# Kernel tuning notes

Measured on AMD Instinct MI355X. Metric: run time of the kernel, lower is better.

## Reference

```python
import jax, jax.numpy as jnp
import numpy as np

B, D, DP, H = 65536, 512, 256, 8
HD = D // H  # head dim = 64
EPS = 1e-5


def _layernorm(x, gamma, beta):
    mu = jnp.mean(x, axis=-1, keepdims=True)
    var = jnp.var(x, axis=-1, keepdims=True)
    return (x - mu) * jax.lax.rsqrt(var + EPS) * gamma + beta


def setup_inputs() -> dict:
    key = jax.random.key(0)
    ks = jax.random.split(key, 16)
    n = lambda k, shape, s=0.02: (jax.random.normal(k, shape, jnp.float32) * s)
    return {
        "cell_emb": jax.random.normal(ks[0], (B, D), jnp.float32),
        "pert_emb": jax.random.normal(ks[1], (B, DP), jnp.float32),
        # perturbation_proj: Linear(DP -> D)
        "Wp": n(ks[2], (D, DP)), "bp": jnp.zeros((D,), jnp.float32),
        # MultiheadAttention in/out projections (each D x D)
        "Wq": n(ks[3], (D, D)), "bq": jnp.zeros((D,), jnp.float32),
        "Wk": n(ks[4], (D, D)), "bk": jnp.zeros((D,), jnp.float32),
        "Wv": n(ks[5], (D, D)), "bv": jnp.zeros((D,), jnp.float32),
        "Wo": n(ks[6], (D, D)), "bo": jnp.zeros((D,), jnp.float32),
        # norm1, norm2
        "g1": jnp.ones((D,), jnp.float32), "be1": jnp.zeros((D,), jnp.float32),
        "g2": jnp.ones((D,), jnp.float32), "be2": jnp.zeros((D,), jnp.float32),
        # FFN: Linear(D -> 2D), GELU, Linear(2D -> D)
        "W1": n(ks[7], (2 * D, D)), "b1": jnp.zeros((2 * D,), jnp.float32),
        "W2": n(ks[8], (D, 2 * D)), "b2": jnp.zeros((D,), jnp.float32),
    }


def reference(cell_emb, pert_emb, Wp, bp, Wq, bq, Wk, bk, Wv, bv, Wo, bo,
              g1, be1, g2, be2, W1, b1, W2, b2):
    # kv = perturbation_proj(pert_emb), length-1 KV sequence
    kv = pert_emb @ Wp.T + bp                       # (B, D)
    # MultiheadAttention with q_len = kv_len = 1
    q = (cell_emb @ Wq.T + bq).reshape(B, H, HD)    # (B, H, HD)
    k = (kv @ Wk.T + bk).reshape(B, H, HD)
    v = (kv @ Wv.T + bv).reshape(B, H, HD)
    # scores over a single key -> softmax yields 1, kept for faithfulness
    logits = jnp.sum(q * k, axis=-1, keepdims=True) / jnp.sqrt(jnp.float32(HD))  # (B, H, 1)
    w = jax.nn.softmax(logits, axis=-1)             # == ones (single key)
    attn = (w * v).reshape(B, D)
    attn_out = attn @ Wo.T + bo                     # (B, D)
    x = _layernorm(cell_emb + attn_out, g1, be1)
    # FFN with exact (erf) GELU, matching torch nn.GELU default
    h = jax.nn.gelu(x @ W1.T + b1, approximate=False)
    ffn_out = h @ W2.T + b2
    return _layernorm(x + ffn_out, g2, be2)
```

## Files before the change

### kernel.cpp

```cpp
#include <hip/hip_runtime.h>
#include <hip/hip_bf16.h>

typedef __bf16 bf16_t;
typedef __attribute__((ext_vector_type(8))) __bf16 bf16x8;
typedef __attribute__((ext_vector_type(4))) float f32x4;

__global__ void prep_wvp(const float* __restrict__ Wv, const float* __restrict__ Wp,
                         const float* __restrict__ bp, const float* __restrict__ bv,
                         float* __restrict__ Wvp, float* __restrict__ bvp) {
  const int i = blockIdx.x;
  const int j = threadIdx.x;
  float a = 0.f;
  for (int d = 0; d < 512; ++d) a += Wv[i * 512 + d] * Wp[d * 256 + j];
  Wvp[i * 256 + j] = a;
  if (j == 0) {
    float b = 0.f;
    for (int d = 0; d < 512; ++d) b += Wv[i * 512 + d] * bp[d];
    bvp[i] = b + bv[i];
  }
}

__global__ void prep_wc(const float* __restrict__ Wo, const float* __restrict__ bo,
                        const float* __restrict__ Wvp, const float* __restrict__ bvp,
                        bf16_t* __restrict__ Wc, float* __restrict__ bcomb) {
  const int o = blockIdx.x;
  const int j = threadIdx.x;
  float a = 0.f;
  for (int i = 0; i < 512; ++i) a += Wo[o * 512 + i] * Wvp[i * 256 + j];
  const int g = o >> 4, rr = o & 15, t = j >> 5, q = (j >> 3) & 3, e = j & 7;
  Wc[((((size_t)g * 8 + t) * 64) + q * 16 + rr) * 8 + e] = (bf16_t)a;
  if (j == 0) {
    float b = 0.f;
    for (int i = 0; i < 512; ++i) b += Wo[o * 512 + i] * bvp[i];
    bcomb[o] = b + bo[o];
  }
}

__global__ void prep_cast(const float* __restrict__ W1, const float* __restrict__ W2,
                          bf16_t* __restrict__ W1b, bf16_t* __restrict__ W2b) {
  const int idx = (blockIdx.x * 256 + threadIdx.x) * 8;
  const float* s;
  bf16_t* d;
  if (idx < 524288) {
    const int o = idx >> 9, k = idx & 511;
    const int g = o >> 4, rr = o & 15, t = k >> 5, q = (k >> 3) & 3;
    s = W1 + idx;
    d = W1b + ((((size_t)g * 16 + t) * 64) + q * 16 + rr) * 8;
  } else {
    const int i2 = idx - 524288;
    const int o = i2 >> 10, k = i2 & 1023;
    const int g = o >> 4, rr = o & 15, t = k >> 5, q = (k >> 3) & 3;
    s = W2 + i2;
    d = W2b + ((((size_t)g * 32 + t) * 64) + q * 16 + rr) * 8;
  }
  float4 u0 = *(const float4*)s;
  float4 u1 = *(const float4*)(s + 4);
  bf16x8 v;
  v[0] = (bf16_t)u0.x; v[1] = (bf16_t)u0.y; v[2] = (bf16_t)u0.z; v[3] = (bf16_t)u0.w;
  v[4] = (bf16_t)u1.x; v[5] = (bf16_t)u1.y; v[6] = (bf16_t)u1.z; v[7] = (bf16_t)u1.w;
  *(bf16x8*)d = v;
}


__device__ __forceinline__ int alay(int row, int k) {
  const int rr = row & 15;
  const int c = (k >> 3) & 3;
  return (((k >> 5) & 15) * 4 + (row >> 4)) * 512 +
         (rr * 4 + (c ^ ((rr >> 1) & 3))) * 8 + (k & 7);
}

template <int STEPS, int NJ>
__device__ __forceinline__ void kloop(const bf16_t* __restrict__ lA_,
                                      const bf16_t* __restrict__ Bp,
                                      int g0, int SB, int soff,
                                      int fRd, int awin, int lane,
                                      f32x4 (&acc)[2][NJ]) {
  constexpr int H = NJ / 2;
  auto bfrag = [&](int j, int s) {
    return *(const bf16x8*)(Bp + ((size_t)((g0 + j) * SB + (soff + s)) * 64 + lane) * 8);
  };
  bf16x8 bA[H], bB[H];
#pragma unroll
  for (int j = 0; j < H; ++j) bA[j] = bfrag(j, 0);
#pragma unroll 2
  for (int s = 0; s < STEPS; ++s) {
#pragma unroll
    for (int j = 0; j < H; ++j) bB[j] = bfrag(H + j, s);
    bf16x8 af[2];
#pragma unroll
    for (int i = 0; i < 2; ++i)
      af[i] = *(const bf16x8*)&lA_[(s * 4 + awin + i) * 512 + fRd];
    __builtin_amdgcn_s_setprio(1);
#pragma unroll
    for (int j = 0; j < H; ++j)
#pragma unroll
      for (int i = 0; i < 2; ++i)
        acc[i][j] = __builtin_amdgcn_mfma_f32_16x16x32_bf16(af[i], bA[j], acc[i][j], 0, 0, 0);
    __builtin_amdgcn_s_setprio(0);
    if (s + 1 < STEPS) {
#pragma unroll
      for (int j = 0; j < H; ++j) bA[j] = bfrag(j, s + 1);
    }
    __builtin_amdgcn_s_setprio(1);
#pragma unroll
    for (int j = 0; j < H; ++j)
#pragma unroll
      for (int i = 0; i < 2; ++i)
        acc[i][H + j] = __builtin_amdgcn_mfma_f32_16x16x32_bf16(af[i], bB[j], acc[i][H + j], 0, 0, 0);
    __builtin_amdgcn_s_setprio(0);
  }
}

__global__ __launch_bounds__(512, 1) void fused_block(
    const float* __restrict__ pert, const bf16_t* __restrict__ Wc,
    const float* __restrict__ bcomb, const float* __restrict__ cell,
    const float* __restrict__ g1, const float* __restrict__ be1,
    const bf16_t* __restrict__ W1b, const float* __restrict__ b1,
    const bf16_t* __restrict__ W2b, const float* __restrict__ b2,
    const float* __restrict__ g2, const float* __restrict__ be2,
    float* __restrict__ out) {

  __shared__ __align__(16) bf16_t lX[64 * 512];
  __shared__ __align__(16) bf16_t lH[64 * 256];
  __shared__ float rs[4][64];
  __shared__ float rss[4][64];

  const int t = threadIdx.x;
  const int m0 = blockIdx.x * 64;
  const int lane = t & 63;
  const int w = t >> 6;
  const int wr = w >> 2;
  const int wc = w & 3;
  const int r = lane & 15;
  const int q = lane >> 4;
  const int qs = q ^ ((r >> 1) & 3);
  const int fRd = r * 32 + qs * 8;
  const int awin = 2 * wr;

#pragma unroll
  for (int u = 0; u < 4; ++u) {
    const int g = u * 512 + t;
    const int row = g >> 5;
    const int c = g & 31;
    const float* src = pert + (size_t)(m0 + row) * 256 + c * 8;
    float4 u0 = *(const float4*)src;
    float4 u1 = *(const float4*)(src + 4);
    bf16x8 v;
    v[0] = (bf16_t)u0.x; v[1] = (bf16_t)u0.y; v[2] = (bf16_t)u0.z; v[3] = (bf16_t)u0.w;
    v[4] = (bf16_t)u1.x; v[5] = (bf16_t)u1.y; v[6] = (bf16_t)u1.z; v[7] = (bf16_t)u1.w;
    *(bf16x8*)&lH[alay(row, c * 8)] = v;
  }
  __syncthreads();

  {
    f32x4 acc1[2][8];
#pragma unroll
    for (int i = 0; i < 2; ++i)
#pragma unroll
      for (int j = 0; j < 8; ++j)
#pragma unroll
        for (int p = 0; p < 4; ++p) acc1[i][j][p] = 0.f;
    kloop<8, 8>(lH, Wc, 8 * wc, 8, 0, fRd, awin, lane, acc1);

    float s_[2][4], ss_[2][4];
#pragma unroll
    for (int i = 0; i < 2; ++i)
#pragma unroll
      for (int p = 0; p < 4; ++p) { s_[i][p] = 0.f; ss_[i][p] = 0.f; }
    float bb[8];
#pragma unroll
    for (int j = 0; j < 8; ++j) bb[j] = bcomb[128 * wc + 16 * j + r];
#pragma unroll
    for (int i = 0; i < 2; ++i)
#pragma unroll
      for (int p = 0; p < 4; ++p) {
        const int rowl = 32 * wr + 16 * i + 4 * q + p;
#pragma unroll
        for (int j = 0; j < 8; ++j) {
          const int col = 128 * wc + 16 * j + r;
          float v = acc1[i][j][p] + bb[j] + cell[(size_t)(m0 + rowl) * 512 + col];
          acc1[i][j][p] = v;
          s_[i][p] += v;
          ss_[i][p] += v * v;
        }
      }
#pragma unroll
    for (int m = 1; m <= 8; m <<= 1)
#pragma unroll
      for (int i = 0; i < 2; ++i)
#pragma unroll
        for (int p = 0; p < 4; ++p) {
          s_[i][p] += __shfl_xor(s_[i][p], m);
          ss_[i][p] += __shfl_xor(ss_[i][p], m);
        }
    if (r == 0) {
#pragma unroll
      for (int i = 0; i < 2; ++i)
#pragma unroll
        for (int p = 0; p < 4; ++p) {
          const int rowl = 32 * wr + 16 * i + 4 * q + p;
          rs[wc][rowl] = s_[i][p];
          rss[wc][rowl] = ss_[i][p];
        }
    }
    __syncthreads();
    float mu[2][4], inv[2][4];
#pragma unroll
    for (int i = 0; i < 2; ++i)
#pragma unroll
      for (int p = 0; p < 4; ++p) {
        const int rowl = 32 * wr + 16 * i + 4 * q + p;
        float tS = rs[0][rowl] + rs[1][rowl] + rs[2][rowl] + rs[3][rowl];
        float tQ = rss[0][rowl] + rss[1][rowl] + rss[2][rowl] + rss[3][rowl];
        float m_ = tS * (1.0f / 512.0f);
        float v_ = tQ * (1.0f / 512.0f) - m_ * m_;
        mu[i][p] = m_;
        inv[i][p] = rsqrtf(v_ + 1e-5f);
      }
    float ga[8], be[8];
#pragma unroll
    for (int j = 0; j < 8; ++j) {
      ga[j] = g1[128 * wc + 16 * j + r];
      be[j] = be1[128 * wc + 16 * j + r];
    }
#pragma unroll
    for (int i = 0; i < 2; ++i)
#pragma unroll
      for (int p = 0; p < 4; ++p) {
        const int rowl = 32 * wr + 16 * i + 4 * q + p;
#pragma unroll
        for (int j = 0; j < 8; ++j) {
          const int col = 128 * wc + 16 * j + r;
          float v = (acc1[i][j][p] - mu[i][p]) * inv[i][p] * ga[j] + be[j];
          lX[alay(rowl, col)] = (bf16_t)v;
        }
      }
  }
  __syncthreads();

  f32x4 acc3[2][8];
#pragma unroll
  for (int i = 0; i < 2; ++i)
#pragma unroll
    for (int j = 0; j < 8; ++j)
#pragma unroll
      for (int p = 0; p < 4; ++p) acc3[i][j][p] = 0.f;

  for (int qh = 0; qh < 4; ++qh) {
    {
      f32x4 accq[2][4];
#pragma unroll
      for (int i = 0; i < 2; ++i)
#pragma unroll
        for (int j = 0; j < 4; ++j)
#pragma unroll
          for (int p = 0; p < 4; ++p) accq[i][j][p] = 0.f;
      kloop<16, 4>(lX, W1b, 16 * qh + 4 * wc, 16, 0, fRd, awin, lane, accq);
      float bb1[4];
#pragma unroll
      for (int j = 0; j < 4; ++j) bb1[j] = b1[256 * qh + 64 * wc + 16 * j + r];
#pragma unroll
      for (int i = 0; i < 2; ++i)
#pragma unroll
        for (int p = 0; p < 4; ++p) {
          const int rowl = 32 * wr + 16 * i + 4 * q + p;
#pragma unroll
          for (int j = 0; j < 4; ++j) {
            const int col = 64 * wc + 16 * j + r;
            float v = accq[i][j][p] + bb1[j];
            float g = 0.5f * v * (1.0f + erff(v * 0.70710678118654752f));
            lH[alay(rowl, col)] = (bf16_t)g;
          }
        }
    }
    __syncthreads();
    kloop<8, 8>(lH, W2b, 8 * wc, 32, 8 * qh, fRd, awin, lane, acc3);
    __syncthreads();
  }

  {
    float s_[2][4], ss_[2][4];
#pragma unroll
    for (int i = 0; i < 2; ++i)
#pragma unroll
      for (int p = 0; p < 4; ++p) { s_[i][p] = 0.f; ss_[i][p] = 0.f; }
    float bb2[8];
#pragma unroll
    for (int j = 0; j < 8; ++j) bb2[j] = b2[128 * wc + 16 * j + r];
#pragma unroll
    for (int i = 0; i < 2; ++i)
#pragma unroll
      for (int p = 0; p < 4; ++p) {
        const int rowl = 32 * wr + 16 * i + 4 * q + p;
#pragma unroll
        for (int j = 0; j < 8; ++j) {
          const int col = 128 * wc + 16 * j + r;
          float v = acc3[i][j][p] + bb2[j] + (float)lX[alay(rowl, col)];
          acc3[i][j][p] = v;
          s_[i][p] += v;
          ss_[i][p] += v * v;
        }
      }
#pragma unroll
    for (int m = 1; m <= 8; m <<= 1)
#pragma unroll
      for (int i = 0; i < 2; ++i)
#pragma unroll
        for (int p = 0; p < 4; ++p) {
          s_[i][p] += __shfl_xor(s_[i][p], m);
          ss_[i][p] += __shfl_xor(ss_[i][p], m);
        }
    __syncthreads();
    if (r == 0) {
#pragma unroll
      for (int i = 0; i < 2; ++i)
#pragma unroll
        for (int p = 0; p < 4; ++p) {
          const int rowl = 32 * wr + 16 * i + 4 * q + p;
          rs[wc][rowl] = s_[i][p];
          rss[wc][rowl] = ss_[i][p];
        }
    }
    __syncthreads();
    float mu[2][4], inv[2][4];
#pragma unroll
    for (int i = 0; i < 2; ++i)
#pragma unroll
      for (int p = 0; p < 4; ++p) {
        const int rowl = 32 * wr + 16 * i + 4 * q + p;
        float tS = rs[0][rowl] + rs[1][rowl] + rs[2][rowl] + rs[3][rowl];
        float tQ = rss[0][rowl] + rss[1][rowl] + rss[2][rowl] + rss[3][rowl];
        float m_ = tS * (1.0f / 512.0f);
        float v_ = tQ * (1.0f / 512.0f) - m_ * m_;
        mu[i][p] = m_;
        inv[i][p] = rsqrtf(v_ + 1e-5f);
      }
    float ga[8], be[8];
#pragma unroll
    for (int j = 0; j < 8; ++j) {
      ga[j] = g2[128 * wc + 16 * j + r];
      be[j] = be2[128 * wc + 16 * j + r];
    }
#pragma unroll
    for (int i = 0; i < 2; ++i)
#pragma unroll
      for (int p = 0; p < 4; ++p) {
        const int rowl = 32 * wr + 16 * i + 4 * q + p;
#pragma unroll
        for (int j = 0; j < 8; ++j) {
          const int col = 128 * wc + 16 * j + r;
          out[(size_t)(m0 + rowl) * 512 + col] =
              (acc3[i][j][p] - mu[i][p]) * inv[i][p] * ga[j] + be[j];
        }
      }
  }
}

extern "C" void kernel_launch(void* const* d_in, const int* in_sizes, int n_in,
                              void* d_out, int out_size, void* d_ws, size_t ws_size,
                              hipStream_t stream) {
  const float* cell = (const float*)d_in[0];
  const float* pert = (const float*)d_in[1];
  const float* Wp   = (const float*)d_in[2];
  const float* bp   = (const float*)d_in[3];
  const float* Wv   = (const float*)d_in[8];
  const float* bv   = (const float*)d_in[9];
  const float* Wo   = (const float*)d_in[10];
  const float* bo   = (const float*)d_in[11];
  const float* g1   = (const float*)d_in[12];
  const float* be1  = (const float*)d_in[13];
  const float* g2   = (const float*)d_in[14];
  const float* be2  = (const float*)d_in[15];
  const float* W1   = (const float*)d_in[16];
  const float* b1   = (const float*)d_in[17];
  const float* W2   = (const float*)d_in[18];
  const float* b2   = (const float*)d_in[19];

  char* ws = (char*)d_ws;
  float*  Wvp   = (float*)(ws + 0);
  float*  bvp   = (float*)(ws + 524288);
  float*  bcomb = (float*)(ws + 526336);
  bf16_t* Wc    = (bf16_t*)(ws + 528384);
  bf16_t* W1b   = (bf16_t*)(ws + 790528);
  bf16_t* W2b   = (bf16_t*)(ws + 1839104);
  (void)in_sizes; (void)n_in; (void)out_size; (void)ws_size;

  prep_wvp<<<512, 256, 0, stream>>>(Wv, Wp, bp, bv, Wvp, bvp);
  prep_wc<<<512, 256, 0, stream>>>(Wo, bo, Wvp, bvp, Wc, bcomb);
  prep_cast<<<512, 256, 0, stream>>>(W1, W2, W1b, W2b);

  fused_block<<<1024, 512, 0, stream>>>(pert, Wc, bcomb, cell, g1, be1,
                                        W1b, b1, W2b, b2, g2, be2,
                                        (float*)d_out);
}
```

Before: 628.7 us.

## Halve row tile to 32 rows with 256-thread blocks, two blocks per CU

Shrinks the fused block from 64 rows with 8 waves (2x4) to 32 rows with 4 waves, doubling the grid and allowing two resident blocks per CU. LDS for X and H is halved and the layernorm reduction scratch is aliased into the lH buffer, which needs an extra barrier before the first stats write. The goal is more independent blocks to overlap the barrier-heavy phases and memory latency. The cost is that each weight fragment fetched from global/L2 is reused across only half as many rows, doubling weight traffic per output row.

Measured after the change: 596.2 us. 1.05x faster.

```diff
diff --git a/kernel.cpp b/kernel.cpp
--- a/kernel.cpp
+++ b/kernel.cpp
@@ -65,7 +65,7 @@
 __device__ __forceinline__ int alay(int row, int k) {
   const int rr = row & 15;
   const int c = (k >> 3) & 3;
-  return (((k >> 5) & 15) * 4 + (row >> 4)) * 512 +
+  return ((k >> 5) * 2 + (row >> 4)) * 512 +
          (rr * 4 + (c ^ ((rr >> 1) & 3))) * 8 + (k & 7);
 }
 
@@ -73,7 +73,7 @@
 __device__ __forceinline__ void kloop(const bf16_t* __restrict__ lA_,
                                       const bf16_t* __restrict__ Bp,
                                       int g0, int SB, int soff,
-                                      int fRd, int awin, int lane,
+                                      int fRd, int lane,
                                       f32x4 (&acc)[2][NJ]) {
   constexpr int H = NJ / 2;
   auto bfrag = [&](int j, int s) {
@@ -89,7 +89,7 @@
     bf16x8 af[2];
 #pragma unroll
     for (int i = 0; i < 2; ++i)
-      af[i] = *(const bf16x8*)&lA_[(s * 4 + awin + i) * 512 + fRd];
+      af[i] = *(const bf16x8*)&lA_[(s * 2 + i) * 512 + fRd];
     __builtin_amdgcn_s_setprio(1);
 #pragma unroll
     for (int j = 0; j < H; ++j)
@@ -111,7 +111,7 @@
   }
 }
 
-__global__ __launch_bounds__(512, 1) void fused_block(
+__global__ __launch_bounds__(256, 2) void fused_block(
     const float* __restrict__ pert, const bf16_t* __restrict__ Wc,
     const float* __restrict__ bcomb, const float* __restrict__ cell,
     const float* __restrict__ g1, const float* __restrict__ be1,
@@ -120,26 +120,23 @@
     const float* __restrict__ g2, const float* __restrict__ be2,
     float* __restrict__ out) {
 
-  __shared__ __align__(16) bf16_t lX[64 * 512];
-  __shared__ __align__(16) bf16_t lH[64 * 256];
-  __shared__ float rs[4][64];
-  __shared__ float rss[4][64];
+  __shared__ __align__(16) bf16_t lX[32 * 512];
+  __shared__ __align__(16) bf16_t lH[32 * 256];
+  float* rsP = (float*)lH;
+  float* ssP = (float*)lH + 128;
 
   const int t = threadIdx.x;
-  const int m0 = blockIdx.x * 64;
+  const int m0 = blockIdx.x * 32;
   const int lane = t & 63;
-  const int w = t >> 6;
-  const int wr = w >> 2;
-  const int wc = w & 3;
+  const int wc = t >> 6;
   const int r = lane & 15;
   const int q = lane >> 4;
   const int qs = q ^ ((r >> 1) & 3);
   const int fRd = r * 32 + qs * 8;
-  const int awin = 2 * wr;
 
 #pragma unroll
   for (int u = 0; u < 4; ++u) {
-    const int g = u * 512 + t;
+    const int g = u * 256 + t;
     const int row = g >> 5;
     const int c = g & 31;
     const float* src = pert + (size_t)(m0 + row) * 256 + c * 8;
@@ -160,7 +157,7 @@
       for (int j = 0; j < 8; ++j)
 #pragma unroll
         for (int p = 0; p < 4; ++p) acc1[i][j][p] = 0.f;
-    kloop<8, 8>(lH, Wc, 8 * wc, 8, 0, fRd, awin, lane, acc1);
+    kloop<8, 8>(lH, Wc, 8 * wc, 8, 0, fRd, lane, acc1);
 
     float s_[2][4], ss_[2][4];
 #pragma unroll
@@ -174,7 +171,7 @@
     for (int i = 0; i < 2; ++i)
 #pragma unroll
       for (int p = 0; p < 4; ++p) {
-        const int rowl = 32 * wr + 16 * i + 4 * q + p;
+        const int rowl = 16 * i + 4 * q + p;
 #pragma unroll
         for (int j = 0; j < 8; ++j) {
           const int col = 128 * wc + 16 * j + r;
@@ -193,14 +190,15 @@
           s_[i][p] += __shfl_xor(s_[i][p], m);
           ss_[i][p] += __shfl_xor(ss_[i][p], m);
         }
+    __syncthreads();
     if (r == 0) {
 #pragma unroll
       for (int i = 0; i < 2; ++i)
 #pragma unroll
         for (int p = 0; p < 4; ++p) {
-          const int rowl = 32 * wr + 16 * i + 4 * q + p;
-          rs[wc][rowl] = s_[i][p];
-          rss[wc][rowl] = ss_[i][p];
+          const int rowl = 16 * i + 4 * q + p;
+          rsP[wc * 32 + rowl] = s_[i][p];
+          ssP[wc * 32 + rowl] = ss_[i][p];
         }
     }
     __syncthreads();
@@ -209,9 +207,9 @@
     for (int i = 0; i < 2; ++i)
 #pragma unroll
       for (int p = 0; p < 4; ++p) {
-        const int rowl = 32 * wr + 16 * i + 4 * q + p;
-        float tS = rs[0][rowl] + rs[1][rowl] + rs[2][rowl] + rs[3][rowl];
-        float tQ = rss[0][rowl] + rss[1][rowl] + rss[2][rowl] + rss[3][rowl];
+        const int rowl = 16 * i + 4 * q + p;
+        float tS = rsP[rowl] + rsP[32 + rowl] + rsP[64 + rowl] + rsP[96 + rowl];
+        float tQ = ssP[rowl] + ssP[32 + rowl] + ssP[64 + rowl] + ssP[96 + rowl];
         float m_ = tS * (1.0f / 512.0f);
         float v_ = tQ * (1.0f / 512.0f) - m_ * m_;
         mu[i][p] = m_;
@@ -227,7 +225,7 @@
     for (int i = 0; i < 2; ++i)
 #pragma unroll
       for (int p = 0; p < 4; ++p) {
-        const int rowl = 32 * wr + 16 * i + 4 * q + p;
+        const int rowl = 16 * i + 4 * q + p;
 #pragma unroll
         for (int j = 0; j < 8; ++j) {
           const int col = 128 * wc + 16 * j + r;
@@ -255,7 +253,7 @@
         for (int j = 0; j < 4; ++j)
 #pragma unroll
           for (int p = 0; p < 4; ++p) accq[i][j][p] = 0.f;
-      kloop<16, 4>(lX, W1b, 16 * qh + 4 * wc, 16, 0, fRd, awin, lane, accq);
+      kloop<16, 4>(lX, W1b, 16 * qh + 4 * wc, 16, 0, fRd, lane, accq);
       float bb1[4];
 #pragma unroll
       for (int j = 0; j < 4; ++j) bb1[j] = b1[256 * qh + 64 * wc + 16 * j + r];
@@ -263,7 +261,7 @@
       for (int i = 0; i < 2; ++i)
 #pragma unroll
         for (int p = 0; p < 4; ++p) {
-          const int rowl = 32 * wr + 16 * i + 4 * q + p;
+          const int rowl = 16 * i + 4 * q + p;
 #pragma unroll
           for (int j = 0; j < 4; ++j) {
             const int col = 64 * wc + 16 * j + r;
@@ -274,7 +272,7 @@
         }
     }
     __syncthreads();
-    kloop<8, 8>(lH, W2b, 8 * wc, 32, 8 * qh, fRd, awin, lane, acc3);
+    kloop<8, 8>(lH, W2b, 8 * wc, 32, 8 * qh, fRd, lane, acc3);
     __syncthreads();
   }
 
@@ -291,7 +289,7 @@
     for (int i = 0; i < 2; ++i)
 #pragma unroll
       for (int p = 0; p < 4; ++p) {
-        const int rowl = 32 * wr + 16 * i + 4 * q + p;
+        const int rowl = 16 * i + 4 * q + p;
 #pragma unroll
         for (int j = 0; j < 8; ++j) {
           const int col = 128 * wc + 16 * j + r;
@@ -310,15 +308,14 @@
           s_[i][p] += __shfl_xor(s_[i][p], m);
           ss_[i][p] += __shfl_xor(ss_[i][p], m);
         }
-    __syncthreads();
     if (r == 0) {
 #pragma unroll
       for (int i = 0; i < 2; ++i)
 #pragma unroll
         for (int p = 0; p < 4; ++p) {
-          const int rowl = 32 * wr + 16 * i + 4 * q + p;
-          rs[wc][rowl] = s_[i][p];
-          rss[wc][rowl] = ss_[i][p];
+          const int rowl = 16 * i + 4 * q + p;
+          rsP[wc * 32 + rowl] = s_[i][p];
+          ssP[wc * 32 + rowl] = ss_[i][p];
         }
     }
     __syncthreads();
@@ -327,9 +324,9 @@
     for (int i = 0; i < 2; ++i)
 #pragma unroll
       for (int p = 0; p < 4; ++p) {
-        const int rowl = 32 * wr + 16 * i + 4 * q + p;
-        float tS = rs[0][rowl] + rs[1][rowl] + rs[2][rowl] + rs[3][rowl];
-        float tQ = rss[0][rowl] + rss[1][rowl] + rss[2][rowl] + rss[3][rowl];
+        const int rowl = 16 * i + 4 * q + p;
+        float tS = rsP[rowl] + rsP[32 + rowl] + rsP[64 + rowl] + rsP[96 + rowl];
+        float tQ = ssP[rowl] + ssP[32 + rowl] + ssP[64 + rowl] + ssP[96 + rowl];
         float m_ = tS * (1.0f / 512.0f);
         float v_ = tQ * (1.0f / 512.0f) - m_ * m_;
         mu[i][p] = m_;
@@ -345,7 +342,7 @@
     for (int i = 0; i < 2; ++i)
 #pragma unroll
       for (int p = 0; p < 4; ++p) {
-        const int rowl = 32 * wr + 16 * i + 4 * q + p;
+        const int rowl = 16 * i + 4 * q + p;
 #pragma unroll
         for (int j = 0; j < 8; ++j) {
           const int col = 128 * wc + 16 * j + r;
@@ -389,7 +386,7 @@
   prep_wc<<<512, 256, 0, stream>>>(Wo, bo, Wvp, bvp, Wc, bcomb);
   prep_cast<<<512, 256, 0, stream>>>(W1, W2, W1b, W2b);
 
-  fused_block<<<1024, 512, 0, stream>>>(pert, Wc, bcomb, cell, g1, be1,
+  fused_block<<<2048, 256, 0, stream>>>(pert, Wc, bcomb, cell, g1, be1,
                                         W1b, b1, W2b, b2, g2, be2,
                                         (float*)d_out);
 }
```
